# Performance work log

Hardware: AMD Instinct MI355X
Metric: run time of the kernel (lower is better)

## Reference

```python
import jax, jax.numpy as jnp
import numpy as np

CHUNKS = 4      # number of segments along in_features
QMAX = 127.0    # int8 symmetric fake quantization
EPS = 1e-8


def fake_quantize(t):
    """Per-tensor symmetric int8 fake quantization with amax scaling (STE-friendly)."""
    amax = jnp.max(jnp.abs(t))
    scale = jnp.maximum(amax / QMAX, EPS)
    q = jnp.clip(jnp.round(t / scale), -QMAX, QMAX) * scale
    # straight-through estimator: identity gradient through the quantizer
    return t + jax.lax.stop_gradient(q - t)


def setup_inputs() -> dict:
    key = jax.random.key(0)
    kx, kw = jax.random.split(key)
    N, K, O = 4096, 4096, 4096  # tokens (B*S), in_features, out_features
    x = jax.random.normal(kx, (N, K), dtype=jnp.float32)
    weight = jax.random.normal(kw, (O, K), dtype=jnp.float32)
    return {"x": x, "weight": weight}


def reference(x, weight):
    # seg_mode='input': split x and weight along in_features into CHUNKS equal chunks,
    # fake-quantize each chunk independently (per-chunk amax scale), run per-chunk
    # GEMMs y_i = fq(x_i) @ fq(w_i)^T and sum over chunks. No bias in 'input' mode.
    N, K = x.shape
    O = weight.shape[0]
    cs = K // CHUNKS
    xc = x.reshape(N, CHUNKS, cs)       # [N, C, cs]
    wc = weight.reshape(O, CHUNKS, cs)  # [O, C, cs]
    fq_chunks = jax.vmap(fake_quantize, in_axes=1, out_axes=1)  # independent amax per chunk
    xq = fq_chunks(xc)
    wq = fq_chunks(wc)
    # sum of per-chunk matmuls == contraction over (chunk, within-chunk) axes
    return jnp.einsum('nck,ock->no', xq, wq)
```

## Files before the change

kernel.cpp:

```cpp
#include <hip/hip_runtime.h>
#include <hip/hip_bf16.h>


constexpr int NDIM = 4096;
constexpr int TOTAL4 = (NDIM * NDIM) / 4;

typedef int i32x4 __attribute__((ext_vector_type(4)));

__global__ __launch_bounds__(256) void amax_kernel(
    const float* __restrict__ x, const float* __restrict__ w,
    unsigned int* __restrict__ amax) {
  const int t = threadIdx.x;
  const int c = blockIdx.x & 3;
  float mx = 0.f, mw = 0.f;
  const float4* x4 = (const float4*)x;
  const float4* w4 = (const float4*)w;
  const int stride = 1024 * 256;
  for (int i = blockIdx.x * 256 + t; i < TOTAL4; i += stride) {
    float4 v = x4[i];
    mx = fmaxf(mx, fmaxf(fmaxf(fabsf(v.x), fabsf(v.y)),
                         fmaxf(fabsf(v.z), fabsf(v.w))));
    float4 u = w4[i];
    mw = fmaxf(mw, fmaxf(fmaxf(fabsf(u.x), fabsf(u.y)),
                         fmaxf(fabsf(u.z), fabsf(u.w))));
  }
  __shared__ float r0[256], r1[256];
  r0[t] = mx; r1[t] = mw;
  __syncthreads();
  for (int off = 128; off; off >>= 1) {
    if (t < off) {
      r0[t] = fmaxf(r0[t], r0[t + off]);
      r1[t] = fmaxf(r1[t], r1[t + off]);
    }
    __syncthreads();
  }
  if (t == 0) {
    atomicMax(&amax[c],     __float_as_uint(r0[0]));
    atomicMax(&amax[4 + c], __float_as_uint(r1[0]));
  }
}

__device__ __forceinline__ signed char quant1(float v, float s) {
  float r = rintf(v / s);
  r = fminf(fmaxf(r, -127.f), 127.f);
  return (signed char)(int)r;
}

__global__ __launch_bounds__(256) void quant_kernel(
    const float* __restrict__ x, const float* __restrict__ w,
    const unsigned int* __restrict__ amax,
    signed char* __restrict__ qx, signed char* __restrict__ qw) {
  const int t = threadIdx.x;
  const int c = blockIdx.x & 3;
  const float sx = fmaxf(__uint_as_float(amax[c])     / 127.0f, 1e-8f);
  const float sw = fmaxf(__uint_as_float(amax[4 + c]) / 127.0f, 1e-8f);
  const float4* x4 = (const float4*)x;
  const float4* w4 = (const float4*)w;
  char4* qx4 = (char4*)qx;
  char4* qw4 = (char4*)qw;
  const int stride = 1024 * 256;
  for (int i = blockIdx.x * 256 + t; i < TOTAL4; i += stride) {
    float4 v = x4[i];
    char4 q;
    q.x = quant1(v.x, sx); q.y = quant1(v.y, sx);
    q.z = quant1(v.z, sx); q.w = quant1(v.w, sx);
    qx4[i] = q;
    float4 u = w4[i];
    char4 p;
    p.x = quant1(u.x, sw); p.y = quant1(u.y, sw);
    p.z = quant1(u.z, sw); p.w = quant1(u.w, sw);
    qw4[i] = p;
  }
}

__device__ __forceinline__ void async16(const void* g, void* l) {
  __builtin_amdgcn_global_load_lds(
      (const __attribute__((address_space(1))) void*)g,
      (__attribute__((address_space(3))) void*)l, 16, 0, 0);
}

__global__ __launch_bounds__(256, 2) void gemm_i8_kernel(
    const signed char* __restrict__ qx, const signed char* __restrict__ qw,
    const unsigned int* __restrict__ amax, float* __restrict__ out) {
  __shared__ __align__(128) signed char lds_a[128 * 64];
  __shared__ __align__(128) signed char lds_b[128 * 64];

  const int t = threadIdx.x;
  const int lane = t & 63;
  const int wave = t >> 6;
  const int brow = blockIdx.y * 128;
  const int bcol = blockIdx.x * 128;
  const int wr = wave >> 1;
  const int wc = wave & 1;

  float scp[4];
#pragma unroll
  for (int c = 0; c < 4; ++c) {
    float sx = fmaxf(__uint_as_float(amax[c])     / 127.0f, 1e-8f);
    float sw = fmaxf(__uint_as_float(amax[4 + c]) / 127.0f, 1e-8f);
    scp[c] = sx * sw;
  }

  const int ar0 = wave * 16 + (lane >> 2);
  const int ar1 = ar0 + 64;
  const int sl = lane & 3;
  const signed char* gax0 = qx + (size_t)(brow + ar0) * NDIM + ((sl ^ (ar0 & 3)) << 4);
  const signed char* gax1 = qx + (size_t)(brow + ar1) * NDIM + ((sl ^ (ar1 & 3)) << 4);
  const signed char* gbx0 = qw + (size_t)(bcol + ar0) * NDIM + ((sl ^ (ar0 & 3)) << 4);
  const signed char* gbx1 = qw + (size_t)(bcol + ar1) * NDIM + ((sl ^ (ar1 & 3)) << 4);
  signed char* lba = &lds_a[wave * 1024];
  signed char* lbb = &lds_b[wave * 1024];

  const int ra = wr * 64 + (lane & 15);
  const int rb = wc * 64 + (lane & 15);
  const int kg = lane >> 4;
  const int offa = ra * 64 + ((kg ^ (ra & 3)) << 4);
  const int offb = rb * 64 + ((kg ^ (rb & 3)) << 4);

  i32x4 iacc[4][4];
  float facc[4][4][4];
#pragma unroll
  for (int m = 0; m < 4; ++m)
#pragma unroll
    for (int n = 0; n < 4; ++n) {
      iacc[m][n] = i32x4{0, 0, 0, 0};
#pragma unroll
      for (int j = 0; j < 4; ++j) facc[m][n][j] = 0.f;
    }

#pragma unroll
  for (int c = 0; c < 4; ++c) {
#pragma unroll 1
    for (int s16 = 0; s16 < 16; ++s16) {
      const int kt = c * 1024 + s16 * 64;
      __syncthreads();
      async16(gax0 + kt, lba);
      async16(gax1 + kt, lba + 4096);
      async16(gbx0 + kt, lbb);
      async16(gbx1 + kt, lbb + 4096);
      __syncthreads();

      i32x4 av[4], bv[4];
#pragma unroll
      for (int m = 0; m < 4; ++m)
        av[m] = *(const i32x4*)&lds_a[offa + m * 16 * 64];
#pragma unroll
      for (int n = 0; n < 4; ++n)
        bv[n] = *(const i32x4*)&lds_b[offb + n * 16 * 64];
#pragma unroll
      for (int m = 0; m < 4; ++m)
#pragma unroll
        for (int n = 0; n < 4; ++n)
          iacc[m][n] = __builtin_amdgcn_mfma_i32_16x16x64_i8(
              av[m], bv[n], iacc[m][n], 0, 0, 0);
    }
    const float s = scp[c];
#pragma unroll
    for (int m = 0; m < 4; ++m)
#pragma unroll
      for (int n = 0; n < 4; ++n) {
#pragma unroll
        for (int j = 0; j < 4; ++j) facc[m][n][j] += s * (float)iacc[m][n][j];
        iacc[m][n] = i32x4{0, 0, 0, 0};
      }
  }

  const int orow = brow + wr * 64 + (lane >> 4) * 4;
  const int ocol = bcol + wc * 64 + (lane & 15);
#pragma unroll
  for (int m = 0; m < 4; ++m)
#pragma unroll
    for (int n = 0; n < 4; ++n)
#pragma unroll
      for (int j = 0; j < 4; ++j)
        out[(size_t)(orow + m * 16 + j) * NDIM + (ocol + n * 16)] = facc[m][n][j];
}

extern "C" void kernel_launch(void* const* d_in, const int* in_sizes, int n_in,
                              void* d_out, int out_size, void* d_ws, size_t ws_size,
                              hipStream_t stream) {
  const float* x = (const float*)d_in[0];
  const float* w = (const float*)d_in[1];
  float* out = (float*)d_out;

  unsigned int* amax = (unsigned int*)d_ws;
  signed char* qx = (signed char*)d_ws + 256;
  signed char* qw = qx + (size_t)NDIM * NDIM;

  hipMemsetAsync(d_ws, 0, 256, stream);
  amax_kernel<<<1024, 256, 0, stream>>>(x, w, amax);
  quant_kernel<<<1024, 256, 0, stream>>>(x, w, amax, qx, qw);
  dim3 grid(NDIM / 128, NDIM / 128);
  gemm_i8_kernel<<<grid, 256, 0, stream>>>(qx, qw, amax, out);
}
```

Measured before the change: 180.9 us.

## Double-buffer LDS tiles in int8 GEMM and swizzle block order

Adds two LDS buffers so the next 64-wide k-tile is loaded asynchronously while the current one feeds MFMAs, halving barriers per tile. Remaps a 1D grid with an interleaved block index to group output tiles for cache locality, and changes the LDS XOR swizzle to use row pairs to reduce bank conflicts. Doubles LDS usage per block, which may affect occupancy at two blocks per CU.

```diff
diff --git a/kernel.cpp b/kernel.cpp
--- a/kernel.cpp
+++ b/kernel.cpp
@@ -82,40 +82,48 @@
 __global__ __launch_bounds__(256, 2) void gemm_i8_kernel(
     const signed char* __restrict__ qx, const signed char* __restrict__ qw,
     const unsigned int* __restrict__ amax, float* __restrict__ out) {
-  __shared__ __align__(128) signed char lds_a[128 * 64];
-  __shared__ __align__(128) signed char lds_b[128 * 64];
+  __shared__ __align__(128) signed char lds_a[2][8192];
+  __shared__ __align__(128) signed char lds_b[2][8192];
 
   const int t = threadIdx.x;
   const int lane = t & 63;
   const int wave = t >> 6;
-  const int brow = blockIdx.y * 128;
-  const int bcol = blockIdx.x * 128;
+
+  const int id = blockIdx.x;
+  const int sid = (id & 7) * 128 + (id >> 3);
+  const int brow = (sid >> 5) * 128;
+  const int bcol = (sid & 31) * 128;
+
   const int wr = wave >> 1;
   const int wc = wave & 1;
 
-  float scp[4];
-#pragma unroll
-  for (int c = 0; c < 4; ++c) {
-    float sx = fmaxf(__uint_as_float(amax[c])     / 127.0f, 1e-8f);
-    float sw = fmaxf(__uint_as_float(amax[4 + c]) / 127.0f, 1e-8f);
-    scp[c] = sx * sw;
+  float s0, s1, s2, s3;
+  {
+    float sx0 = fmaxf(__uint_as_float(amax[0]) / 127.0f, 1e-8f);
+    float sx1 = fmaxf(__uint_as_float(amax[1]) / 127.0f, 1e-8f);
+    float sx2 = fmaxf(__uint_as_float(amax[2]) / 127.0f, 1e-8f);
+    float sx3 = fmaxf(__uint_as_float(amax[3]) / 127.0f, 1e-8f);
+    float sw0 = fmaxf(__uint_as_float(amax[4]) / 127.0f, 1e-8f);
+    float sw1 = fmaxf(__uint_as_float(amax[5]) / 127.0f, 1e-8f);
+    float sw2 = fmaxf(__uint_as_float(amax[6]) / 127.0f, 1e-8f);
+    float sw3 = fmaxf(__uint_as_float(amax[7]) / 127.0f, 1e-8f);
+    s0 = sx0 * sw0; s1 = sx1 * sw1; s2 = sx2 * sw2; s3 = sx3 * sw3;
   }
 
   const int ar0 = wave * 16 + (lane >> 2);
   const int ar1 = ar0 + 64;
   const int sl = lane & 3;
-  const signed char* gax0 = qx + (size_t)(brow + ar0) * NDIM + ((sl ^ (ar0 & 3)) << 4);
-  const signed char* gax1 = qx + (size_t)(brow + ar1) * NDIM + ((sl ^ (ar1 & 3)) << 4);
-  const signed char* gbx0 = qw + (size_t)(bcol + ar0) * NDIM + ((sl ^ (ar0 & 3)) << 4);
-  const signed char* gbx1 = qw + (size_t)(bcol + ar1) * NDIM + ((sl ^ (ar1 & 3)) << 4);
-  signed char* lba = &lds_a[wave * 1024];
-  signed char* lbb = &lds_b[wave * 1024];
+  const signed char* gax0 = qx + (size_t)(brow + ar0) * NDIM + ((sl ^ ((ar0 >> 1) & 3)) << 4);
+  const signed char* gax1 = qx + (size_t)(brow + ar1) * NDIM + ((sl ^ ((ar1 >> 1) & 3)) << 4);
+  const signed char* gbx0 = qw + (size_t)(bcol + ar0) * NDIM + ((sl ^ ((ar0 >> 1) & 3)) << 4);
+  const signed char* gbx1 = qw + (size_t)(bcol + ar1) * NDIM + ((sl ^ ((ar1 >> 1) & 3)) << 4);
+  const int ldsoff = wave * 1024;
 
   const int ra = wr * 64 + (lane & 15);
   const int rb = wc * 64 + (lane & 15);
   const int kg = lane >> 4;
-  const int offa = ra * 64 + ((kg ^ (ra & 3)) << 4);
-  const int offb = rb * 64 + ((kg ^ (rb & 3)) << 4);
+  const int offa = ra * 64 + ((kg ^ ((ra >> 1) & 3)) << 4);
+  const int offb = rb * 64 + ((kg ^ ((rb >> 1) & 3)) << 4);
 
   i32x4 iacc[4][4];
   float facc[4][4][4];
@@ -128,42 +136,59 @@
       for (int j = 0; j < 4; ++j) facc[m][n][j] = 0.f;
     }
 
-#pragma unroll
-  for (int c = 0; c < 4; ++c) {
+#define STAGE(BUF, T)                                        \
+  do {                                                       \
+    const int kt_ = (T) * 64;                                \
+    async16(gax0 + kt_, &lds_a[BUF][ldsoff]);                \
+    async16(gax1 + kt_, &lds_a[BUF][ldsoff + 4096]);         \
+    async16(gbx0 + kt_, &lds_b[BUF][ldsoff]);                \
+    async16(gbx1 + kt_, &lds_b[BUF][ldsoff + 4096]);         \
+  } while (0)
+
+#define COMPUTE(BUF)                                                    \
+  do {                                                                  \
+    i32x4 av[4], bv[4];                                                 \
+    _Pragma("unroll")                                                   \
+    for (int m = 0; m < 4; ++m)                                         \
+      av[m] = *(const i32x4*)&lds_a[BUF][offa + m * 1024];              \
+    _Pragma("unroll")                                                   \
+    for (int n = 0; n < 4; ++n)                                         \
+      bv[n] = *(const i32x4*)&lds_b[BUF][offb + n * 1024];              \
+    _Pragma("unroll")                                                   \
+    for (int m = 0; m < 4; ++m)                                         \
+      _Pragma("unroll")                                                 \
+      for (int n = 0; n < 4; ++n)                                       \
+        iacc[m][n] = __builtin_amdgcn_mfma_i32_16x16x64_i8(             \
+            av[m], bv[n], iacc[m][n], 0, 0, 0);                         \
+  } while (0)
+
+#define FOLD(S)                                                         \
+  do {                                                                  \
+    _Pragma("unroll")                                                   \
+    for (int m = 0; m < 4; ++m)                                         \
+      _Pragma("unroll")                                                 \
+      for (int n = 0; n < 4; ++n) {                                     \
+        _Pragma("unroll")                                               \
+        for (int j = 0; j < 4; ++j) facc[m][n][j] += (S) * (float)iacc[m][n][j]; \
+        iacc[m][n] = i32x4{0, 0, 0, 0};                                 \
+      }                                                                 \
+  } while (0)
+
+  STAGE(0, 0);
 #pragma unroll 1
-    for (int s16 = 0; s16 < 16; ++s16) {
-      const int kt = c * 1024 + s16 * 64;
-      __syncthreads();
-      async16(gax0 + kt, lba);
-      async16(gax1 + kt, lba + 4096);
-      async16(gbx0 + kt, lbb);
-      async16(gbx1 + kt, lbb + 4096);
-      __syncthreads();
-
-      i32x4 av[4], bv[4];
-#pragma unroll
-      for (int m = 0; m < 4; ++m)
-        av[m] = *(const i32x4*)&lds_a[offa + m * 16 * 64];
-#pragma unroll
-      for (int n = 0; n < 4; ++n)
-        bv[n] = *(const i32x4*)&lds_b[offb + n * 16 * 64];
-#pragma unroll
-      for (int m = 0; m < 4; ++m)
-#pragma unroll
-        for (int n = 0; n < 4; ++n)
-          iacc[m][n] = __builtin_amdgcn_mfma_i32_16x16x64_i8(
-              av[m], bv[n], iacc[m][n], 0, 0, 0);
-    }
-    const float s = scp[c];
-#pragma unroll
-    for (int m = 0; m < 4; ++m)
-#pragma unroll
-      for (int n = 0; n < 4; ++n) {
-#pragma unroll
-        for (int j = 0; j < 4; ++j) facc[m][n][j] += s * (float)iacc[m][n][j];
-        iacc[m][n] = i32x4{0, 0, 0, 0};
-      }
-  }
+  for (int tp = 0; tp < 32; ++tp) {
+    const int t1 = 2 * tp + 1;
+    __syncthreads();
+    STAGE(1, t1);
+    COMPUTE(0);
+    __syncthreads();
+    if (t1 < 63) STAGE(0, t1 + 1);
+    COMPUTE(1);
+    if (t1 == 15) FOLD(s0);
+    else if (t1 == 31) FOLD(s1);
+    else if (t1 == 47) FOLD(s2);
+  }
+  FOLD(s3);
 
   const int orow = brow + wr * 64 + (lane >> 4) * 4;
   const int ocol = bcol + wc * 64 + (lane & 15);
@@ -174,6 +199,9 @@
 #pragma unroll
       for (int j = 0; j < 4; ++j)
         out[(size_t)(orow + m * 16 + j) * NDIM + (ocol + n * 16)] = facc[m][n][j];
+#undef STAGE
+#undef COMPUTE
+#undef FOLD
 }
 
 extern "C" void kernel_launch(void* const* d_in, const int* in_sizes, int n_in,
@@ -190,6 +218,5 @@
   hipMemsetAsync(d_ws, 0, 256, stream);
   amax_kernel<<<1024, 256, 0, stream>>>(x, w, amax);
   quant_kernel<<<1024, 256, 0, stream>>>(x, w, amax, qx, qw);
-  dim3 grid(NDIM / 128, NDIM / 128);
-  gemm_i8_kernel<<<grid, 256, 0, stream>>>(qx, qw, amax, out);
-}
+  gemm_i8_kernel<<<1024, 256, 0, stream>>>(qx, qw, amax, out);
+}
```

Result: slower. 288.9 us (+59.8%).
